# Kernel tuning notes

Hardware: AMD Instinct MI355X
Metric: run time of the kernel (lower is better)

The kernel has to match this reference:

```python
import jax, jax.numpy as jnp
import numpy as np

N, E = 50000, 800000
IN_D, HID, H1, OUT_D, H2, EDGE_D = 64, 16, 8, 64, 2, 1
NEG_SLOPE = 0.2


def gatv2_layer(x, src, dst, edge_attr, Wl, Wr, We, att, bias, concat):
    """PyG GATv2Conv (add_self_loops=False, share_weights=False), eval mode (no dropout)."""
    n = x.shape[0]
    H, C = att.shape
    xl = (x @ Wl).reshape(n, H, C)            # source transform
    xr = (x @ Wr).reshape(n, H, C)            # target transform
    ee = (edge_attr @ We).reshape(-1, H, C)   # edge embedding
    z = jax.nn.leaky_relu(xl[src] + xr[dst] + ee, NEG_SLOPE)  # [E,H,C]
    score = jnp.einsum('ehc,hc->eh', z, att)                  # [E,H]
    # softmax over incoming edges per target node
    m = jax.ops.segment_max(score, dst, num_segments=n)
    m = jnp.where(jnp.isfinite(m), m, 0.0)
    a = jnp.exp(score - m[dst])
    denom = jax.ops.segment_sum(a, dst, num_segments=n)
    alpha = a / (denom[dst] + 1e-16)                          # [E,H]
    msg = xl[src] * alpha[..., None]                          # [E,H,C]
    out = jax.ops.segment_sum(msg, dst, num_segments=n)       # [N,H,C]
    if concat:
        return out.reshape(n, H * C) + bias
    return out.mean(axis=1) + bias


def layer_norm(x, g, b):
    mu = x.mean(-1, keepdims=True)
    var = ((x - mu) ** 2).mean(-1, keepdims=True)
    return (x - mu) * jax.lax.rsqrt(var + 1e-5) * g + b


def setup_inputs() -> dict:
    key = jax.random.key(0)
    ks = jax.random.split(key, 24)
    def w(k, *shape):
        fan_in = shape[0]
        return jax.random.normal(k, shape, dtype=jnp.float32) * (1.0 / np.sqrt(fan_in))
    inp = {
        'x': jax.random.normal(ks[0], (N, IN_D), dtype=jnp.float32),
        'edge_index': jax.random.randint(ks[1], (2, E), 0, N, dtype=jnp.int64),
        'edge_attr': jax.random.normal(ks[2], (E, EDGE_D), dtype=jnp.float32),
        # layer 1 (heads=8, out=16, concat)
        'w1_l': w(ks[3], IN_D, H1 * HID), 'w1_r': w(ks[4], IN_D, H1 * HID),
        'w1_e': w(ks[5], EDGE_D, H1 * HID),
        'att1': jax.random.normal(ks[6], (H1, HID), dtype=jnp.float32) * 0.1,
        'b1': jnp.zeros((H1 * HID,), dtype=jnp.float32),
        # layer 2 (heads=2, out=64, mean)
        'w2_l': w(ks[7], H1 * HID, H2 * OUT_D), 'w2_r': w(ks[8], H1 * HID, H2 * OUT_D),
        'w2_e': w(ks[9], EDGE_D, H2 * OUT_D),
        'att2': jax.random.normal(ks[10], (H2, OUT_D), dtype=jnp.float32) * 0.1,
        'b2': jnp.zeros((OUT_D,), dtype=jnp.float32),
        # classifier: Linear + LayerNorm + GELU + ResidualBlockv2
        'wc': w(ks[11], OUT_D, OUT_D), 'bc': jnp.zeros((OUT_D,), dtype=jnp.float32),
        'ln_g': jnp.ones((OUT_D,), dtype=jnp.float32), 'ln_b': jnp.zeros((OUT_D,), dtype=jnp.float32),
        'wr': w(ks[12], OUT_D, OUT_D), 'br': jnp.zeros((OUT_D,), dtype=jnp.float32),
        'lnr_g': jnp.ones((OUT_D,), dtype=jnp.float32), 'lnr_b': jnp.zeros((OUT_D,), dtype=jnp.float32),
    }
    return inp


def reference(x, edge_index, edge_attr, w1_l, w1_r, w1_e, att1, b1,
              w2_l, w2_r, w2_e, att2, b2, wc, bc, ln_g, ln_b, wr, br, lnr_g, lnr_b):
    src, dst = edge_index[0], edge_index[1]
    h = jax.nn.relu(gatv2_layer(x, src, dst, edge_attr, w1_l, w1_r, w1_e, att1, b1, True))
    h = jax.nn.relu(gatv2_layer(h, src, dst, edge_attr, w2_l, w2_r, w2_e, att2, b2, False))
    h = jax.nn.gelu(layer_norm(h @ wc + bc, ln_g, ln_b), approximate=False)
    # ResidualBlockv2: Linear -> LayerNorm -> GELU with residual skip
    h = h + jax.nn.gelu(layer_norm(h @ wr + br, lnr_g, lnr_b), approximate=False)
    return h
```

## Files before the change

kernel.cpp:

```cpp
#include <hip/hip_runtime.h>
#include <math.h>

#define NNODE 50000
#define NEDGE 800000
#define NBLK_SCAN 196

__device__ __forceinline__ float wsum64(float v) {
    #pragma unroll
    for (int m = 32; m >= 1; m >>= 1) v += __shfl_xor(v, m, 64);
    return v;
}

__device__ __forceinline__ float gelu_exact(float x) {
    return 0.5f * x * (1.0f + erff(x * 0.70710678118654752f));
}

__device__ __forceinline__ float lrelu(float z) { return z > 0.f ? z : 0.2f * z; }

__global__ void fill_u32(unsigned* __restrict__ p, unsigned v, int n) {
    int i = blockIdx.x * blockDim.x + threadIdx.x;
    if (i < n) p[i] = v;
}

__global__ __launch_bounds__(256) void build_deg(const int* __restrict__ ei, int* __restrict__ deg) {
    int e = blockIdx.x * 256 + threadIdx.x;
    if (e >= NEDGE) return;
    atomicAdd(&deg[ei[NEDGE + e]], 1);
}

__global__ __launch_bounds__(256) void scan1(const int* __restrict__ deg,
                                             int* __restrict__ partial,
                                             int* __restrict__ bsum) {
    __shared__ int tmp[256];
    int t = threadIdx.x;
    int gid = blockIdx.x * 256 + t;
    int v = (gid < NNODE) ? deg[gid] : 0;
    tmp[t] = v;
    __syncthreads();
    #pragma unroll
    for (int off = 1; off < 256; off <<= 1) {
        int u = (t >= off) ? tmp[t - off] : 0;
        __syncthreads();
        tmp[t] += u;
        __syncthreads();
    }
    if (gid < NNODE) partial[gid] = tmp[t] - v;
    if (t == 255) bsum[blockIdx.x] = tmp[255];
}

__global__ __launch_bounds__(256) void scan2(int* __restrict__ bsum, int* __restrict__ boff) {
    __shared__ int tmp[256];
    int t = threadIdx.x;
    int v = (t < NBLK_SCAN) ? bsum[t] : 0;
    tmp[t] = v;
    __syncthreads();
    #pragma unroll
    for (int off = 1; off < 256; off <<= 1) {
        int u = (t >= off) ? tmp[t - off] : 0;
        __syncthreads();
        tmp[t] += u;
        __syncthreads();
    }
    if (t < NBLK_SCAN) boff[t] = tmp[t] - v;
}

__global__ __launch_bounds__(256) void scan3(const int* __restrict__ partial,
                                             const int* __restrict__ boff,
                                             int* __restrict__ base,
                                             int* __restrict__ cursor) {
    int gid = blockIdx.x * 256 + threadIdx.x;
    if (gid < NNODE) {
        int b = partial[gid] + boff[blockIdx.x];
        base[gid] = b;
        cursor[gid] = b;
    }
    if (gid == 0) base[NNODE] = NEDGE;
}

__global__ __launch_bounds__(256) void scatter_edges(const int* __restrict__ ei,
                                                     const float* __restrict__ ea,
                                                     int* __restrict__ cursor,
                                                     int2* __restrict__ se) {
    int e = blockIdx.x * 256 + threadIdx.x;
    if (e >= NEDGE) return;
    int d = ei[NEDGE + e];
    int i = atomicAdd(&cursor[d], 1);
    se[i] = make_int2(ei[e], __float_as_int(ea[e]));
}

template<int K>
__global__ __launch_bounds__(256) void node_xform(const float* __restrict__ in,
                                                  const float* __restrict__ wl,
                                                  const float* __restrict__ wr,
                                                  float* __restrict__ xl,
                                                  float* __restrict__ xr) {
    __shared__ float xrow[32][K];
    int t = threadIdx.x;
    int n0 = blockIdx.x * 32;
    for (int idx = t; idx < 32 * (K / 4); idx += 256) {
        int row = idx / (K / 4), c4 = idx % (K / 4);
        float4 v = make_float4(0.f, 0.f, 0.f, 0.f);
        if (n0 + row < NNODE) v = ((const float4*)(in + (size_t)(n0 + row) * K))[c4];
        ((float4*)xrow[row])[c4] = v;
    }
    __syncthreads();
    int cg = t & 63, ns = t >> 6;
    const float* wsel = (cg < 32) ? wl : wr;
    float* osel = (cg < 32) ? xl : xr;
    int ccol = (cg & 31) * 4;
    const float* wp = wsel + ccol;
    const float* xbase = xrow[ns * 8];
    float4 acc[8];
    #pragma unroll
    for (int k = 0; k < 8; ++k) acc[k] = make_float4(0.f, 0.f, 0.f, 0.f);
    for (int i = 0; i < K; i += 4) {
        float4 w0 = *(const float4*)(wp + (size_t)(i + 0) * 128);
        float4 w1 = *(const float4*)(wp + (size_t)(i + 1) * 128);
        float4 w2 = *(const float4*)(wp + (size_t)(i + 2) * 128);
        float4 w3 = *(const float4*)(wp + (size_t)(i + 3) * 128);
        #pragma unroll
        for (int k = 0; k < 8; ++k) {
            float4 xv = *(const float4*)(xbase + (size_t)k * K + i);
            acc[k].x += xv.x * w0.x + xv.y * w1.x + xv.z * w2.x + xv.w * w3.x;
            acc[k].y += xv.x * w0.y + xv.y * w1.y + xv.z * w2.y + xv.w * w3.y;
            acc[k].z += xv.x * w0.z + xv.y * w1.z + xv.z * w2.z + xv.w * w3.z;
            acc[k].w += xv.x * w0.w + xv.y * w1.w + xv.z * w2.w + xv.w * w3.w;
        }
    }
    #pragma unroll
    for (int k = 0; k < 8; ++k) {
        int n = n0 + ns * 8 + k;
        if (n < NNODE) *(float4*)(osel + (size_t)n * 128 + ccol) = acc[k];
    }
}

__global__ __launch_bounds__(256) void fused1(const int* __restrict__ base,
                                              const int2* __restrict__ se,
                                              const float* __restrict__ xl,
                                              const float* __restrict__ xr,
                                              const float* __restrict__ w1e,
                                              const float* __restrict__ att1,
                                              const float* __restrict__ b1,
                                              float* __restrict__ h1) {
    int t = threadIdx.x;
    int wv = t >> 6, ln = t & 63;
    int half = ln >> 5, sub = ln & 31;
    int n = blockIdx.x * 4 + wv;
    int ch = sub * 4;
    float4 xrv = *(const float4*)(xr + (size_t)n * 128 + ch);
    float4 wev = *(const float4*)(w1e + ch);
    float4 atv = *(const float4*)(att1 + ch);
    int i0 = base[n], i1 = base[n + 1];
    float m = -1e30f, den = 0.f;
    float4 o = make_float4(0.f, 0.f, 0.f, 0.f);
    int i = i0 + half;
    if (i < i1) {
        int2 r = se[i];
        float4 xv = *(const float4*)(xl + (size_t)r.x * 128 + ch);
        float a = __int_as_float(r.y);
        for (i += 2; i < i1; i += 2) {
            int2 rn = se[i];
            float4 nxv = *(const float4*)(xl + (size_t)rn.x * 128 + ch);
            float na = __int_as_float(rn.y);
            float part = lrelu(fmaf(a, wev.x, xv.x + xrv.x)) * atv.x
                       + lrelu(fmaf(a, wev.y, xv.y + xrv.y)) * atv.y
                       + lrelu(fmaf(a, wev.z, xv.z + xrv.z)) * atv.z
                       + lrelu(fmaf(a, wev.w, xv.w + xrv.w)) * atv.w;
            part += __shfl_xor(part, 1, 64);
            part += __shfl_xor(part, 2, 64);
            float mn = fmaxf(m, part);
            float sc = __expf(m - mn);
            float p  = __expf(part - mn);
            den = den * sc + p;
            o.x = o.x * sc + p * xv.x;
            o.y = o.y * sc + p * xv.y;
            o.z = o.z * sc + p * xv.z;
            o.w = o.w * sc + p * xv.w;
            m = mn;
            xv = nxv; a = na;
        }
        float part = lrelu(fmaf(a, wev.x, xv.x + xrv.x)) * atv.x
                   + lrelu(fmaf(a, wev.y, xv.y + xrv.y)) * atv.y
                   + lrelu(fmaf(a, wev.z, xv.z + xrv.z)) * atv.z
                   + lrelu(fmaf(a, wev.w, xv.w + xrv.w)) * atv.w;
        part += __shfl_xor(part, 1, 64);
        part += __shfl_xor(part, 2, 64);
        float mn = fmaxf(m, part);
        float sc = __expf(m - mn);
        float p  = __expf(part - mn);
        den = den * sc + p;
        o.x = o.x * sc + p * xv.x;
        o.y = o.y * sc + p * xv.y;
        o.z = o.z * sc + p * xv.z;
        o.w = o.w * sc + p * xv.w;
        m = mn;
    }
    float m2   = __shfl_xor(m, 32, 64);
    float den2 = __shfl_xor(den, 32, 64);
    float4 o2;
    o2.x = __shfl_xor(o.x, 32, 64);
    o2.y = __shfl_xor(o.y, 32, 64);
    o2.z = __shfl_xor(o.z, 32, 64);
    o2.w = __shfl_xor(o.w, 32, 64);
    float mn = fmaxf(m, m2);
    float s1 = __expf(m - mn), s2 = __expf(m2 - mn);
    den = den * s1 + den2 * s2;
    float inv = 1.f / (den + 1e-16f);
    if (half == 0) {
        float4 bv = *(const float4*)(b1 + ch);
        float4 res;
        res.x = fmaxf((o.x * s1 + o2.x * s2) * inv + bv.x, 0.f);
        res.y = fmaxf((o.y * s1 + o2.y * s2) * inv + bv.y, 0.f);
        res.z = fmaxf((o.z * s1 + o2.z * s2) * inv + bv.z, 0.f);
        res.w = fmaxf((o.w * s1 + o2.w * s2) * inv + bv.w, 0.f);
        *(float4*)(h1 + (size_t)n * 128 + ch) = res;
    }
}

__global__ __launch_bounds__(256) void fused2(const int* __restrict__ base,
                                              const int2* __restrict__ se,
                                              const float* __restrict__ xl,
                                              const float* __restrict__ xr,
                                              const float* __restrict__ w2e,
                                              const float* __restrict__ att2,
                                              const float* __restrict__ b2,
                                              float* __restrict__ h2) {
    int t = threadIdx.x;
    int wv = t >> 6, ln = t & 63;
    int half = ln >> 5, sub = ln & 31;
    int n = blockIdx.x * 4 + wv;
    int ch = sub * 4;
    float4 xrv = *(const float4*)(xr + (size_t)n * 128 + ch);
    float4 wev = *(const float4*)(w2e + ch);
    float4 atv = *(const float4*)(att2 + ch);
    int i0 = base[n], i1 = base[n + 1];
    float m = -1e30f, den = 0.f;
    float4 o = make_float4(0.f, 0.f, 0.f, 0.f);
    int i = i0 + half;
    if (i < i1) {
        int2 r = se[i];
        float4 xv = *(const float4*)(xl + (size_t)r.x * 128 + ch);
        float a = __int_as_float(r.y);
        for (i += 2; i < i1; i += 2) {
            int2 rn = se[i];
            float4 nxv = *(const float4*)(xl + (size_t)rn.x * 128 + ch);
            float na = __int_as_float(rn.y);
            float part = lrelu(fmaf(a, wev.x, xv.x + xrv.x)) * atv.x
                       + lrelu(fmaf(a, wev.y, xv.y + xrv.y)) * atv.y
                       + lrelu(fmaf(a, wev.z, xv.z + xrv.z)) * atv.z
                       + lrelu(fmaf(a, wev.w, xv.w + xrv.w)) * atv.w;
            part += __shfl_xor(part, 1, 64);
            part += __shfl_xor(part, 2, 64);
            part += __shfl_xor(part, 4, 64);
            part += __shfl_xor(part, 8, 64);
            float mn = fmaxf(m, part);
            float sc = __expf(m - mn);
            float p  = __expf(part - mn);
            den = den * sc + p;
            o.x = o.x * sc + p * xv.x;
            o.y = o.y * sc + p * xv.y;
            o.z = o.z * sc + p * xv.z;
            o.w = o.w * sc + p * xv.w;
            m = mn;
            xv = nxv; a = na;
        }
        float part = lrelu(fmaf(a, wev.x, xv.x + xrv.x)) * atv.x
                   + lrelu(fmaf(a, wev.y, xv.y + xrv.y)) * atv.y
                   + lrelu(fmaf(a, wev.z, xv.z + xrv.z)) * atv.z
                   + lrelu(fmaf(a, wev.w, xv.w + xrv.w)) * atv.w;
        part += __shfl_xor(part, 1, 64);
        part += __shfl_xor(part, 2, 64);
        part += __shfl_xor(part, 4, 64);
        part += __shfl_xor(part, 8, 64);
        float mn = fmaxf(m, part);
        float sc = __expf(m - mn);
        float p  = __expf(part - mn);
        den = den * sc + p;
        o.x = o.x * sc + p * xv.x;
        o.y = o.y * sc + p * xv.y;
        o.z = o.z * sc + p * xv.z;
        o.w = o.w * sc + p * xv.w;
        m = mn;
    }
    float m2   = __shfl_xor(m, 32, 64);
    float den2 = __shfl_xor(den, 32, 64);
    float4 o2;
    o2.x = __shfl_xor(o.x, 32, 64);
    o2.y = __shfl_xor(o.y, 32, 64);
    o2.z = __shfl_xor(o.z, 32, 64);
    o2.w = __shfl_xor(o.w, 32, 64);
    float mn = fmaxf(m, m2);
    float s1 = __expf(m - mn), s2 = __expf(m2 - mn);
    den = den * s1 + den2 * s2;
    float inv = 1.f / (den + 1e-16f);
    float4 v;
    v.x = (o.x * s1 + o2.x * s2) * inv;
    v.y = (o.y * s1 + o2.y * s2) * inv;
    v.z = (o.z * s1 + o2.z * s2) * inv;
    v.w = (o.w * s1 + o2.w * s2) * inv;
    float4 u;
    u.x = __shfl_xor(v.x, 16, 64);
    u.y = __shfl_xor(v.y, 16, 64);
    u.z = __shfl_xor(v.z, 16, 64);
    u.w = __shfl_xor(v.w, 16, 64);
    if (half == 0 && sub < 16) {
        float4 bv = *(const float4*)(b2 + ch);
        float4 res;
        res.x = fmaxf(0.5f * (v.x + u.x) + bv.x, 0.f);
        res.y = fmaxf(0.5f * (v.y + u.y) + bv.y, 0.f);
        res.z = fmaxf(0.5f * (v.z + u.z) + bv.z, 0.f);
        res.w = fmaxf(0.5f * (v.w + u.w) + bv.w, 0.f);
        *(float4*)(h2 + (size_t)n * 64 + ch) = res;
    }
}

__global__ __launch_bounds__(256) void classifier(const float* __restrict__ h2,
                                                  const float* __restrict__ wc,
                                                  const float* __restrict__ bc,
                                                  const float* __restrict__ lng,
                                                  const float* __restrict__ lnb,
                                                  const float* __restrict__ wr,
                                                  const float* __restrict__ br,
                                                  const float* __restrict__ lrg,
                                                  const float* __restrict__ lrb,
                                                  float* __restrict__ out) {
    __shared__ float rowA[4][64];
    __shared__ float rowB[4][64];
    int t = threadIdx.x;
    int wv = t >> 6, ln = t & 63;
    int n = blockIdx.x * 4 + wv;
    rowA[wv][ln] = h2[(size_t)n * 64 + ln];
    __syncthreads();
    float acc = bc[ln];
    #pragma unroll 8
    for (int i = 0; i < 64; ++i) acc += rowA[wv][i] * wc[i * 64 + ln];
    float mu = wsum64(acc) * (1.f / 64.f);
    float dv = acc - mu;
    float var = wsum64(dv * dv) * (1.f / 64.f);
    float y = dv * rsqrtf(var + 1e-5f) * lng[ln] + lnb[ln];
    float g1 = gelu_exact(y);
    rowB[wv][ln] = g1;
    __syncthreads();
    float acc2 = br[ln];
    #pragma unroll 8
    for (int i = 0; i < 64; ++i) acc2 += rowB[wv][i] * wr[i * 64 + ln];
    float mu2 = wsum64(acc2) * (1.f / 64.f);
    float dv2 = acc2 - mu2;
    float var2 = wsum64(dv2 * dv2) * (1.f / 64.f);
    float y2 = dv2 * rsqrtf(var2 + 1e-5f) * lrg[ln] + lrb[ln];
    float g2 = gelu_exact(y2);
    out[(size_t)n * 64 + ln] = g1 + g2;
}

extern "C" void kernel_launch(void* const* d_in, const int* in_sizes, int n_in,
                              void* d_out, int out_size, void* d_ws, size_t ws_size,
                              hipStream_t stream) {
    const float* x    = (const float*)d_in[0];
    const int*   ei   = (const int*)d_in[1];
    const float* ea   = (const float*)d_in[2];
    const float* w1l  = (const float*)d_in[3];
    const float* w1r  = (const float*)d_in[4];
    const float* w1e  = (const float*)d_in[5];
    const float* att1 = (const float*)d_in[6];
    const float* b1   = (const float*)d_in[7];
    const float* w2l  = (const float*)d_in[8];
    const float* w2r  = (const float*)d_in[9];
    const float* w2e  = (const float*)d_in[10];
    const float* att2 = (const float*)d_in[11];
    const float* b2   = (const float*)d_in[12];
    const float* wc   = (const float*)d_in[13];
    const float* bc   = (const float*)d_in[14];
    const float* lng  = (const float*)d_in[15];
    const float* lnb  = (const float*)d_in[16];
    const float* wr   = (const float*)d_in[17];
    const float* br   = (const float*)d_in[18];
    const float* lrg  = (const float*)d_in[19];
    const float* lrb  = (const float*)d_in[20];

    float* ws = (float*)d_ws;
    const size_t N128 = (size_t)NNODE * 128;
    float* xl = ws;
    float* xr = xl + N128;
    float* h1 = xr + N128;
    float* h2 = h1 + N128;
    int2*  se      = (int2*)(h2 + (size_t)NNODE * 64);
    int*   deg     = (int*)(se + NEDGE);
    int*   partial = deg + NNODE;
    int*   base    = partial + NNODE;
    int*   cursor  = base + NNODE + 1;
    int*   bsum    = cursor + NNODE;
    int*   boff    = bsum + 256;

    const int EB  = NEDGE / 256;
    const int NBX = (NNODE + 31) / 32;
    const int NB4 = NNODE / 4;

    fill_u32<<<NBLK_SCAN, 256, 0, stream>>>((unsigned*)deg, 0u, NNODE);
    build_deg<<<EB, 256, 0, stream>>>(ei, deg);
    scan1<<<NBLK_SCAN, 256, 0, stream>>>(deg, partial, bsum);
    scan2<<<1, 256, 0, stream>>>(bsum, boff);
    scan3<<<NBLK_SCAN, 256, 0, stream>>>(partial, boff, base, cursor);
    scatter_edges<<<EB, 256, 0, stream>>>(ei, ea, cursor, se);

    node_xform<64><<<NBX, 256, 0, stream>>>(x, w1l, w1r, xl, xr);
    fused1<<<NB4, 256, 0, stream>>>(base, se, xl, xr, w1e, att1, b1, h1);

    node_xform<128><<<NBX, 256, 0, stream>>>(h1, w2l, w2r, xl, xr);
    fused2<<<NB4, 256, 0, stream>>>(base, se, xl, xr, w2e, att2, b2, h2);

    classifier<<<NB4, 256, 0, stream>>>(h2, wc, bc, lng, lnb, wr, br, lrg, lrb,
                                        (float*)d_out);
}
```

Baseline: 351.6 us.

## Fuse classifier into layer-2 aggregation and collapse scan into one kernel

The layer-2 GATv2 aggregation now writes its output row into shared memory, and the classifier MLP with its LayerNorm and GELU stages runs in the same kernel. This removes the h2 global buffer round trip and one launch. The three-kernel degree scan becomes a single-block kernel in which each thread serially scans a contiguous chunk. That cuts launches but serialises the work on one CU with uncoalesced per-thread reads.

```diff
diff --git a/kernel.cpp b/kernel.cpp
--- a/kernel.cpp
+++ b/kernel.cpp
@@ -3,7 +3,7 @@
 
 #define NNODE 50000
 #define NEDGE 800000
-#define NBLK_SCAN 196
+#define NBLK 196
 
 __device__ __forceinline__ float wsum64(float v) {
     #pragma unroll
@@ -28,53 +28,32 @@
     atomicAdd(&deg[ei[NEDGE + e]], 1);
 }
 
-__global__ __launch_bounds__(256) void scan1(const int* __restrict__ deg,
-                                             int* __restrict__ partial,
-                                             int* __restrict__ bsum) {
-    __shared__ int tmp[256];
+__global__ __launch_bounds__(256) void scan_all(const int* __restrict__ deg,
+                                                int* __restrict__ base,
+                                                int* __restrict__ cursor) {
+    __shared__ int tsum[256];
     int t = threadIdx.x;
-    int gid = blockIdx.x * 256 + t;
-    int v = (gid < NNODE) ? deg[gid] : 0;
-    tmp[t] = v;
+    const int CH = (NNODE + 255) / 256;
+    int s0 = t * CH, s1 = min(s0 + CH, NNODE);
+    int s = 0;
+    for (int i = s0; i < s1; ++i) s += deg[i];
+    tsum[t] = s;
     __syncthreads();
     #pragma unroll
     for (int off = 1; off < 256; off <<= 1) {
-        int u = (t >= off) ? tmp[t - off] : 0;
+        int u = (t >= off) ? tsum[t - off] : 0;
         __syncthreads();
-        tmp[t] += u;
+        tsum[t] += u;
         __syncthreads();
     }
-    if (gid < NNODE) partial[gid] = tmp[t] - v;
-    if (t == 255) bsum[blockIdx.x] = tmp[255];
-}
-
-__global__ __launch_bounds__(256) void scan2(int* __restrict__ bsum, int* __restrict__ boff) {
-    __shared__ int tmp[256];
-    int t = threadIdx.x;
-    int v = (t < NBLK_SCAN) ? bsum[t] : 0;
-    tmp[t] = v;
-    __syncthreads();
-    #pragma unroll
-    for (int off = 1; off < 256; off <<= 1) {
-        int u = (t >= off) ? tmp[t - off] : 0;
-        __syncthreads();
-        tmp[t] += u;
-        __syncthreads();
-    }
-    if (t < NBLK_SCAN) boff[t] = tmp[t] - v;
-}
-
-__global__ __launch_bounds__(256) void scan3(const int* __restrict__ partial,
-                                             const int* __restrict__ boff,
-                                             int* __restrict__ base,
-                                             int* __restrict__ cursor) {
-    int gid = blockIdx.x * 256 + threadIdx.x;
-    if (gid < NNODE) {
-        int b = partial[gid] + boff[blockIdx.x];
-        base[gid] = b;
-        cursor[gid] = b;
-    }
-    if (gid == 0) base[NNODE] = NEDGE;
+    int run = tsum[t] - s;
+    for (int i = s0; i < s1; ++i) {
+        int d = deg[i];
+        base[i] = run;
+        cursor[i] = run;
+        run += d;
+    }
+    if (t == 0) base[NNODE] = NEDGE;
 }
 
 __global__ __launch_bounds__(256) void scatter_edges(const int* __restrict__ ei,
@@ -217,14 +196,24 @@
     }
 }
 
-__global__ __launch_bounds__(256) void fused2(const int* __restrict__ base,
-                                              const int2* __restrict__ se,
-                                              const float* __restrict__ xl,
-                                              const float* __restrict__ xr,
-                                              const float* __restrict__ w2e,
-                                              const float* __restrict__ att2,
-                                              const float* __restrict__ b2,
-                                              float* __restrict__ h2) {
+__global__ __launch_bounds__(256) void fused2cls(const int* __restrict__ base,
+                                                 const int2* __restrict__ se,
+                                                 const float* __restrict__ xl,
+                                                 const float* __restrict__ xr,
+                                                 const float* __restrict__ w2e,
+                                                 const float* __restrict__ att2,
+                                                 const float* __restrict__ b2,
+                                                 const float* __restrict__ wc,
+                                                 const float* __restrict__ bc,
+                                                 const float* __restrict__ lng,
+                                                 const float* __restrict__ lnb,
+                                                 const float* __restrict__ wrr,
+                                                 const float* __restrict__ brr,
+                                                 const float* __restrict__ lrg,
+                                                 const float* __restrict__ lrb,
+                                                 float* __restrict__ out) {
+    __shared__ float rowH[4][64];
+    __shared__ float rowB[4][64];
     int t = threadIdx.x;
     int wv = t >> 6, ln = t & 63;
     int half = ln >> 5, sub = ln & 31;
@@ -310,30 +299,12 @@
         res.y = fmaxf(0.5f * (v.y + u.y) + bv.y, 0.f);
         res.z = fmaxf(0.5f * (v.z + u.z) + bv.z, 0.f);
         res.w = fmaxf(0.5f * (v.w + u.w) + bv.w, 0.f);
-        *(float4*)(h2 + (size_t)n * 64 + ch) = res;
-    }
-}
-
-__global__ __launch_bounds__(256) void classifier(const float* __restrict__ h2,
-                                                  const float* __restrict__ wc,
-                                                  const float* __restrict__ bc,
-                                                  const float* __restrict__ lng,
-                                                  const float* __restrict__ lnb,
-                                                  const float* __restrict__ wr,
-                                                  const float* __restrict__ br,
-                                                  const float* __restrict__ lrg,
-                                                  const float* __restrict__ lrb,
-                                                  float* __restrict__ out) {
-    __shared__ float rowA[4][64];
-    __shared__ float rowB[4][64];
-    int t = threadIdx.x;
-    int wv = t >> 6, ln = t & 63;
-    int n = blockIdx.x * 4 + wv;
-    rowA[wv][ln] = h2[(size_t)n * 64 + ln];
+        *(float4*)(&rowH[wv][ch]) = res;
+    }
     __syncthreads();
     float acc = bc[ln];
     #pragma unroll 8
-    for (int i = 0; i < 64; ++i) acc += rowA[wv][i] * wc[i * 64 + ln];
+    for (int j = 0; j < 64; ++j) acc += rowH[wv][j] * wc[j * 64 + ln];
     float mu = wsum64(acc) * (1.f / 64.f);
     float dv = acc - mu;
     float var = wsum64(dv * dv) * (1.f / 64.f);
@@ -341,9 +312,9 @@
     float g1 = gelu_exact(y);
     rowB[wv][ln] = g1;
     __syncthreads();
-    float acc2 = br[ln];
+    float acc2 = brr[ln];
     #pragma unroll 8
-    for (int i = 0; i < 64; ++i) acc2 += rowB[wv][i] * wr[i * 64 + ln];
+    for (int j = 0; j < 64; ++j) acc2 += rowB[wv][j] * wrr[j * 64 + ln];
     float mu2 = wsum64(acc2) * (1.f / 64.f);
     float dv2 = acc2 - mu2;
     float var2 = wsum64(dv2 * dv2) * (1.f / 64.f);
@@ -382,32 +353,25 @@
     float* xl = ws;
     float* xr = xl + N128;
     float* h1 = xr + N128;
-    float* h2 = h1 + N128;
-    int2*  se      = (int2*)(h2 + (size_t)NNODE * 64);
+    int2*  se      = (int2*)(h1 + N128);
     int*   deg     = (int*)(se + NEDGE);
-    int*   partial = deg + NNODE;
-    int*   base    = partial + NNODE;
+    int*   base    = deg + NNODE;
     int*   cursor  = base + NNODE + 1;
-    int*   bsum    = cursor + NNODE;
-    int*   boff    = bsum + 256;
 
     const int EB  = NEDGE / 256;
     const int NBX = (NNODE + 31) / 32;
     const int NB4 = NNODE / 4;
 
-    fill_u32<<<NBLK_SCAN, 256, 0, stream>>>((unsigned*)deg, 0u, NNODE);
+    fill_u32<<<NBLK, 256, 0, stream>>>((unsigned*)deg, 0u, NNODE);
     build_deg<<<EB, 256, 0, stream>>>(ei, deg);
-    scan1<<<NBLK_SCAN, 256, 0, stream>>>(deg, partial, bsum);
-    scan2<<<1, 256, 0, stream>>>(bsum, boff);
-    scan3<<<NBLK_SCAN, 256, 0, stream>>>(partial, boff, base, cursor);
+    scan_all<<<1, 256, 0, stream>>>(deg, base, cursor);
     scatter_edges<<<EB, 256, 0, stream>>>(ei, ea, cursor, se);
 
     node_xform<64><<<NBX, 256, 0, stream>>>(x, w1l, w1r, xl, xr);
     fused1<<<NB4, 256, 0, stream>>>(base, se, xl, xr, w1e, att1, b1, h1);
 
     node_xform<128><<<NBX, 256, 0, stream>>>(h1, w2l, w2r, xl, xr);
-    fused2<<<NB4, 256, 0, stream>>>(base, se, xl, xr, w2e, att2, b2, h2);
-
-    classifier<<<NB4, 256, 0, stream>>>(h2, wc, bc, lng, lnb, wr, br, lrg, lrb,
-                                        (float*)d_out);
-}
+    fused2cls<<<NB4, 256, 0, stream>>>(base, se, xl, xr, w2e, att2, b2,
+                                       wc, bc, lng, lnb, wr, br, lrg, lrb,
+                                       (float*)d_out);
+}
```

After: 452.0 us. 1.29x slower.
